# Optimization experiments

Hardware: AMD Instinct MI355X
Metric: run time of the kernel (lower is better)

Reference implementation:

```python
import jax, jax.numpy as jnp
import numpy as np

B, L, D = 2, 4096, 128      # batch, seq_len, d_model
ED = 2 * D                  # d_inner (expand=2) = 256
N = 16                      # d_state
K = 4                       # d_conv
R = (D + 15) // 16          # dt_rank = 8
H = 2 * D                   # mlp hidden = 256


def setup_inputs() -> dict:
    key = jax.random.key(0)
    ks = jax.random.split(key, 20)
    s = 0.05
    inp = {
        "x": jax.random.normal(ks[0], (B, L, D), dtype=jnp.float32),
        # outer block LayerNorm (norm1)
        "norm1_g": jnp.ones((D,), jnp.float32),
        "norm1_b": jnp.zeros((D,), jnp.float32),
        # MambaLayer inner LayerNorm
        "inner_g": jnp.ones((D,), jnp.float32),
        "inner_b": jnp.zeros((D,), jnp.float32),
        # Mamba params
        "in_w": jax.random.normal(ks[1], (2 * ED, D), jnp.float32) * s,      # in_proj (no bias)
        "conv_w": jax.random.normal(ks[2], (ED, 1, K), jnp.float32) * s,     # depthwise conv
        "conv_b": jax.random.normal(ks[3], (ED,), jnp.float32) * s,
        "xproj_w": jax.random.normal(ks[4], (R + 2 * N, ED), jnp.float32) * s,  # x_proj (no bias)
        "dt_w": jax.random.normal(ks[5], (ED, R), jnp.float32) * s,
        "dt_b": jax.random.normal(ks[6], (ED,), jnp.float32) * s,
        "A_log": jnp.tile(jnp.log(jnp.arange(1, N + 1, dtype=jnp.float32)), (ED, 1)),  # [ED,N]
        "Dp": jnp.ones((ED,), jnp.float32),
        "out_w": jax.random.normal(ks[7], (D, ED), jnp.float32) * s,         # out_proj (no bias)
        # MLP
        "fc1_w": jax.random.normal(ks[8], (H, D), jnp.float32) * s,
        "fc1_b": jnp.zeros((H,), jnp.float32),
        "fc2_w": jax.random.normal(ks[9], (D, H), jnp.float32) * s,
        "fc2_b": jnp.zeros((D,), jnp.float32),
    }
    return inp


def _ln(x, g, b, eps=1e-5):
    m = jnp.mean(x, axis=-1, keepdims=True)
    v = jnp.mean((x - m) ** 2, axis=-1, keepdims=True)
    return (x - m) * jax.lax.rsqrt(v + eps) * g + b


def _mamba(x, in_w, conv_w, conv_b, xproj_w, dt_w, dt_b, A_log, Dp, out_w):
    # x: [B, L, D]
    xz = jnp.einsum('bld,ed->ble', x, in_w)          # [B,L,2*ED]
    u, z = jnp.split(xz, 2, axis=-1)                 # each [B,L,ED]
    # causal depthwise conv1d over L
    u_c = jnp.transpose(u, (0, 2, 1))                # [B,ED,L]
    u_c = jax.lax.conv_general_dilated(
        u_c, conv_w, window_strides=(1,), padding=[(K - 1, 0)],
        dimension_numbers=('NCH', 'OIH', 'NCH'), feature_group_count=ED)
    u = jax.nn.silu(jnp.transpose(u_c, (0, 2, 1)) + conv_b)   # [B,L,ED]
    # input-dependent dt, B, C
    dbc = jnp.einsum('ble,re->blr', u, xproj_w)      # [B,L,R+2N]
    dt, Bm, Cm = jnp.split(dbc, [R, R + N], axis=-1)
    delta = jax.nn.softplus(jnp.einsum('blr,er->ble', dt, dt_w) + dt_b)  # [B,L,ED]
    A = -jnp.exp(A_log)                              # [ED,N]
    deltaA = jnp.exp(jnp.einsum('ble,en->blen', delta, A))               # [B,L,ED,N]
    deltaBu = jnp.einsum('ble,bln,ble->blen', delta, Bm, u)              # [B,L,ED,N]
    # selective scan over L
    def step(h, inp):
        dA, dBu, Ct = inp                            # [B,ED,N],[B,ED,N],[B,N]
        h = dA * h + dBu
        y = jnp.einsum('ben,bn->be', h, Ct)
        return h, y
    h0 = jnp.zeros((B, ED, N), u.dtype)
    xs = (jnp.transpose(deltaA, (1, 0, 2, 3)),
          jnp.transpose(deltaBu, (1, 0, 2, 3)),
          jnp.transpose(Cm, (1, 0, 2)))
    _, ys = jax.lax.scan(step, h0, xs)               # [L,B,ED]
    y = jnp.transpose(ys, (1, 0, 2)) + u * Dp        # [B,L,ED]
    y = y * jax.nn.silu(z)
    return jnp.einsum('ble,de->bld', y, out_w)       # [B,L,D]


def reference(x, norm1_g, norm1_b, inner_g, inner_b, in_w, conv_w, conv_b,
              xproj_w, dt_w, dt_b, A_log, Dp, out_w, fc1_w, fc1_b, fc2_w, fc2_b):
    # attn branch: mamba(inner_LN(norm1(x)))
    a = _mamba(_ln(_ln(x, norm1_g, norm1_b), inner_g, inner_b),
               in_w, conv_w, conv_b, xproj_w, dt_w, dt_b, A_log, Dp, out_w)
    x = x + a
    # mlp branch (note: original applies norm1 again to updated x)
    h = _ln(x, norm1_g, norm1_b)
    h = jax.nn.gelu(jnp.einsum('bld,hd->blh', h, fc1_w) + fc1_b, approximate=False)
    h = jnp.einsum('blh,dh->bld', h, fc2_w) + fc2_b
    return x + h
```

## Files before the change

kernel.cpp:

```cpp
#include <hip/hip_runtime.h>
#include <hip/hip_bf16.h>
#include <math.h>

#define BB 2
#define LL 4096
#define DD 128
#define ED 256
#define NN 16
#define KK 4
#define RR 8
#define HH 256
#define NT (BB*LL)
#define NC 128
#define LC 32

typedef __attribute__((ext_vector_type(8))) short short8;
typedef __attribute__((ext_vector_type(8))) unsigned short ushort8v;
typedef __attribute__((ext_vector_type(4))) float floatx4;

__device__ __forceinline__ unsigned short f2bf(float f) {
  unsigned int b = __builtin_bit_cast(unsigned int, f);
  b += 0x7FFFu + ((b >> 16) & 1u);
  return (unsigned short)(b >> 16);
}

__device__ __forceinline__ ushort8v pack8(const float4& v0, const float4& v1) {
  ushort8v p;
  p[0]=f2bf(v0.x); p[1]=f2bf(v0.y); p[2]=f2bf(v0.z); p[3]=f2bf(v0.w);
  p[4]=f2bf(v1.x); p[5]=f2bf(v1.y); p[6]=f2bf(v1.z); p[7]=f2bf(v1.w);
  return p;
}

__global__ __launch_bounds__(256) void gemm_inln_k(const float* __restrict__ x,
    const float* __restrict__ g1, const float* __restrict__ b1,
    const float* __restrict__ g2, const float* __restrict__ b2,
    const float* __restrict__ W, float* __restrict__ C) {
  __shared__ unsigned short As[64][136];
  __shared__ unsigned short Ws[64][136];
  const int row0 = blockIdx.y * 64;
  const int col0 = blockIdx.x * 64;
  const int tid  = threadIdx.x;
  const int wave = tid >> 6, lane = tid & 63;
  const int quad = lane >> 4, l16 = lane & 15;
  const int wm = (wave & 1) * 32, wn = (wave >> 1) * 32;
  const int lr = tid >> 2;
  const int lk = (tid & 3) * 32;

  {
    const float* Ap = x + (size_t)(row0 + lr)*DD + lk;
    float4 av[8];
    float s = 0.f, sq = 0.f;
    #pragma unroll
    for (int g = 0; g < 8; g++) {
      av[g] = *(const float4*)(Ap + g*4);
      s  += av[g].x + av[g].y + av[g].z + av[g].w;
      sq += av[g].x*av[g].x + av[g].y*av[g].y + av[g].z*av[g].z + av[g].w*av[g].w;
    }
    s += __shfl_xor(s, 1);  s += __shfl_xor(s, 2);
    sq += __shfl_xor(sq, 1); sq += __shfl_xor(sq, 2);
    const float m1 = s * (1.f/128.f);
    const float rs1 = rsqrtf(sq*(1.f/128.f) - m1*m1 + 1e-5f);
    float s2 = 0.f, sq2 = 0.f;
    #pragma unroll
    for (int g = 0; g < 8; g++) {
      const float4 gg = *(const float4*)(g1 + lk + g*4);
      const float4 bb = *(const float4*)(b1 + lk + g*4);
      av[g].x = (av[g].x - m1)*rs1*gg.x + bb.x;
      av[g].y = (av[g].y - m1)*rs1*gg.y + bb.y;
      av[g].z = (av[g].z - m1)*rs1*gg.z + bb.z;
      av[g].w = (av[g].w - m1)*rs1*gg.w + bb.w;
      s2  += av[g].x + av[g].y + av[g].z + av[g].w;
      sq2 += av[g].x*av[g].x + av[g].y*av[g].y + av[g].z*av[g].z + av[g].w*av[g].w;
    }
    s2 += __shfl_xor(s2, 1);  s2 += __shfl_xor(s2, 2);
    sq2 += __shfl_xor(sq2, 1); sq2 += __shfl_xor(sq2, 2);
    const float m2 = s2 * (1.f/128.f);
    const float rs2 = rsqrtf(sq2*(1.f/128.f) - m2*m2 + 1e-5f);
    #pragma unroll
    for (int g = 0; g < 4; g++) {
      const float4 ga = *(const float4*)(g2 + lk + g*8);
      const float4 gb = *(const float4*)(g2 + lk + g*8 + 4);
      const float4 ba = *(const float4*)(b2 + lk + g*8);
      const float4 bbv= *(const float4*)(b2 + lk + g*8 + 4);
      ushort8v pa;
      pa[0] = f2bf((av[2*g].x   - m2)*rs2*ga.x + ba.x);
      pa[1] = f2bf((av[2*g].y   - m2)*rs2*ga.y + ba.y);
      pa[2] = f2bf((av[2*g].z   - m2)*rs2*ga.z + ba.z);
      pa[3] = f2bf((av[2*g].w   - m2)*rs2*ga.w + ba.w);
      pa[4] = f2bf((av[2*g+1].x - m2)*rs2*gb.x + bbv.x);
      pa[5] = f2bf((av[2*g+1].y - m2)*rs2*gb.y + bbv.y);
      pa[6] = f2bf((av[2*g+1].z - m2)*rs2*gb.z + bbv.z);
      pa[7] = f2bf((av[2*g+1].w - m2)*rs2*gb.w + bbv.w);
      *(ushort8v*)&As[lr][lk + g*8] = pa;
    }
  }
  {
    const float* Wp = W + (size_t)(col0 + lr)*DD + lk;
    #pragma unroll
    for (int g = 0; g < 4; g++) {
      const float4 v0 = *(const float4*)(Wp + g*8);
      const float4 v1 = *(const float4*)(Wp + g*8 + 4);
      *(ushort8v*)&Ws[lr][lk + g*8] = pack8(v0, v1);
    }
  }
  __syncthreads();

  floatx4 acc[2][2] = {};
  #pragma unroll
  for (int ks = 0; ks < 4; ks++) {
    const int ko = ks*32 + quad*8;
    short8 a0 = *(const short8*)&As[wm +      l16][ko];
    short8 a1 = *(const short8*)&As[wm + 16 + l16][ko];
    short8 b0 = *(const short8*)&Ws[wn +      l16][ko];
    short8 b1 = *(const short8*)&Ws[wn + 16 + l16][ko];
    acc[0][0] = __builtin_amdgcn_mfma_f32_16x16x32_bf16(a0, b0, acc[0][0], 0, 0, 0);
    acc[0][1] = __builtin_amdgcn_mfma_f32_16x16x32_bf16(a0, b1, acc[0][1], 0, 0, 0);
    acc[1][0] = __builtin_amdgcn_mfma_f32_16x16x32_bf16(a1, b0, acc[1][0], 0, 0, 0);
    acc[1][1] = __builtin_amdgcn_mfma_f32_16x16x32_bf16(a1, b1, acc[1][1], 0, 0, 0);
  }
  #pragma unroll
  for (int i = 0; i < 2; i++)
    #pragma unroll
    for (int j = 0; j < 2; j++) {
      const int n = col0 + wn + j*16 + l16;
      #pragma unroll
      for (int r = 0; r < 4; r++) {
        const int m = row0 + wm + i*16 + quad*4 + r;
        C[(size_t)m*(2*ED) + n] = acc[i][j][r];
      }
    }
}

__global__ __launch_bounds__(256) void scan1f_k(
    const float* __restrict__ xz, const float* __restrict__ cw,
    const float* __restrict__ cb, const float* __restrict__ xpw,
    const float* __restrict__ dtw, const float* __restrict__ dtb,
    const float* __restrict__ A_log, float* __restrict__ uc,
    float* __restrict__ dbc, float* __restrict__ delta,
    float* __restrict__ cA, float* __restrict__ cH) {
  __shared__ __align__(16) unsigned short Bs[64][264];
  __shared__ __align__(16) unsigned short As[32][264];
  __shared__ float su[32][128];
  __shared__ float sdbc[32][40];
  float (*sdel)[128] = reinterpret_cast<float(*)[128]>(&As[0][0]);

  const int eb = blockIdx.x, c = blockIdx.y, b = blockIdx.z;
  const int tid = threadIdx.x;
  const int t0 = b*LL + c*LC;

  #pragma unroll
  for (int p = 0; p < 8; p++) {
    const int idx = p*256 + tid;
    const int row = idx >> 5;
    const int col = (idx & 31) * 8;
    ushort8v v = {};
    if (row < 40) {
      const float4 v0 = *(const float4*)(xpw + (size_t)row*ED + col);
      const float4 v1 = *(const float4*)(xpw + (size_t)row*ED + col + 4);
      v = pack8(v0, v1);
    }
    *(ushort8v*)&Bs[row][col] = v;
  }

  {
    const int ch = tid;
    const float4 w = *(const float4*)(cw + ch*4);
    const float cbe = cb[ch];
    float h0 = 0.f, h1 = 0.f, h2 = 0.f;
    if (c != 0) {
      h0 = xz[(size_t)(t0-3)*(2*ED) + ch];
      h1 = xz[(size_t)(t0-2)*(2*ED) + ch];
      h2 = xz[(size_t)(t0-1)*(2*ED) + ch];
    }
    const bool own = (ch >> 7) == eb;
    #pragma unroll 8
    for (int i = 0; i < LC; i++) {
      const float cur = xz[(size_t)(t0+i)*(2*ED) + ch];
      const float a = cbe + h0*w.x + h1*w.y + h2*w.z + cur*w.w;
      const float s = a / (1.f + __expf(-a));
      As[i][ch] = f2bf(s);
      if (own) {
        su[i][ch & 127] = s;
        uc[(size_t)(t0+i)*ED + ch] = s;
      }
      h0 = h1; h1 = h2; h2 = cur;
    }
  }
  __syncthreads();

  const int wave = tid >> 6, lane = tid & 63;
  const int quad = lane >> 4, l16 = lane & 15;
  {
    const int mi = (wave & 1) * 16;
    const int j0 = (wave >> 1) * 2;
    floatx4 acc[2] = {};
    #pragma unroll
    for (int ks = 0; ks < 8; ks++) {
      const int ko = ks*32 + quad*8;
      short8 a  = *(const short8*)&As[mi + l16][ko];
      short8 b0 = *(const short8*)&Bs[j0*16 +      l16][ko];
      short8 b1 = *(const short8*)&Bs[j0*16 + 16 + l16][ko];
      acc[0] = __builtin_amdgcn_mfma_f32_16x16x32_bf16(a, b0, acc[0], 0, 0, 0);
      acc[1] = __builtin_amdgcn_mfma_f32_16x16x32_bf16(a, b1, acc[1], 0, 0, 0);
    }
    __syncthreads();
    #pragma unroll
    for (int f = 0; f < 2; f++) {
      const int n = (j0 + f)*16 + l16;
      #pragma unroll
      for (int r = 0; r < 4; r++) {
        const int m = mi + quad*4 + r;
        if (n < 40) {
          sdbc[m][n] = acc[f][r];
          if (eb == 0) dbc[(size_t)(t0 + m)*40 + n] = acc[f][r];
        }
      }
    }
  }
  __syncthreads();

  const int e_loc = tid >> 1;
  const int half  = tid & 1;
  const int e     = eb*128 + e_loc;
  {
    const float4 w0 = *(const float4*)(dtw + e*RR);
    const float4 w1 = *(const float4*)(dtw + e*RR + 4);
    const float db = dtb[e];
    #pragma unroll 4
    for (int i = 0; i < 16; i++) {
      const int t = half*16 + i;
      const float a = db
          + sdbc[t][0]*w0.x + sdbc[t][1]*w0.y + sdbc[t][2]*w0.z + sdbc[t][3]*w0.w
          + sdbc[t][4]*w1.x + sdbc[t][5]*w1.y + sdbc[t][6]*w1.z + sdbc[t][7]*w1.w;
      const float d = (a > 20.f) ? a : log1pf(__expf(a));
      sdel[t][e_loc] = d;
      delta[(size_t)(t0+t)*ED + e] = d;
    }
  }
  __syncthreads();

  const int n0 = half * 8;
  const float4 a0 = *(const float4*)(A_log + e*NN + n0);
  const float4 a1 = *(const float4*)(A_log + e*NN + n0 + 4);
  float Aen[8] = {-__expf(a0.x), -__expf(a0.y), -__expf(a0.z), -__expf(a0.w),
                  -__expf(a1.x), -__expf(a1.y), -__expf(a1.z), -__expf(a1.w)};
  float h[8] = {};
  float sumd = 0.f;
  for (int i = 0; i < LC; i++) {
    const float dv = sdel[i][e_loc];
    const float du = dv * su[i][e_loc];
    const float4 B0 = *(const float4*)&sdbc[i][RR + n0];
    const float4 B1 = *(const float4*)&sdbc[i][RR + n0 + 4];
    const float Bv[8] = {B0.x,B0.y,B0.z,B0.w,B1.x,B1.y,B1.z,B1.w};
    sumd += dv;
    #pragma unroll
    for (int j = 0; j < 8; j++)
      h[j] = __expf(dv * Aen[j])*h[j] + Bv[j]*du;
  }
  const size_t base = (((size_t)c*BB + b)*ED + e)*NN + n0;
  *(float4*)(cA + base)     = make_float4(__expf(sumd*Aen[0]), __expf(sumd*Aen[1]),
                                          __expf(sumd*Aen[2]), __expf(sumd*Aen[3]));
  *(float4*)(cA + base + 4) = make_float4(__expf(sumd*Aen[4]), __expf(sumd*Aen[5]),
                                          __expf(sumd*Aen[6]), __expf(sumd*Aen[7]));
  *(float4*)(cH + base)     = make_float4(h[0], h[1], h[2], h[3]);
  *(float4*)(cH + base + 4) = make_float4(h[4], h[5], h[6], h[7]);
}

__global__ __launch_bounds__(256) void scan2_k(float* __restrict__ cA,
    const float* __restrict__ cH) {
  const int gt = blockIdx.x*256 + threadIdx.x;
  const int b = gt >> 12;
  const size_t base = (size_t)b*ED*NN + (gt & 4095);
  float h = 0.f;
  for (int g = 0; g < NC/16; g++) {
    float av[16], hv[16];
    #pragma unroll
    for (int i = 0; i < 16; i++) {
      const size_t idx = (size_t)(g*16 + i)*(BB*ED*NN) + base;
      av[i] = cA[idx]; hv[i] = cH[idx];
    }
    #pragma unroll
    for (int i = 0; i < 16; i++) {
      const size_t idx = (size_t)(g*16 + i)*(BB*ED*NN) + base;
      cA[idx] = h;
      h = av[i]*h + hv[i];
    }
  }
}

__global__ __launch_bounds__(256, 1) void tail_k(
    const float* __restrict__ xz, const float* __restrict__ delta,
    const float* __restrict__ uc, const float* __restrict__ dbc,
    const float* __restrict__ cP, const float* __restrict__ A_log,
    const float* __restrict__ Dpv, const float* __restrict__ x,
    const float* __restrict__ g1, const float* __restrict__ b1,
    const float* __restrict__ out_w, const float* __restrict__ fc1_w,
    const float* __restrict__ fc1_b, const float* __restrict__ fc2_w,
    const float* __restrict__ fc2_b, float* __restrict__ out) {
  __shared__ __align__(16) unsigned short BigW[34816];
  __shared__ __align__(16) unsigned short Au[32][264];
  __shared__ float xs[32][132];
  __shared__ float sbc[32][32];

  const int c = blockIdx.x, b = blockIdx.y;
  const int t0 = b*LL + c*LC;
  const int tid = threadIdx.x;
  const int wave = tid >> 6, lane = tid & 63;
  const int quad = lane >> 4, l16 = lane & 15;

  #pragma unroll
  for (int p = 0; p < 4; p++) {
    const int idx = p*256 + tid;
    const int row = idx >> 5, col = idx & 31;
    sbc[row][col] = dbc[(size_t)(t0 + row)*40 + RR + col];
  }

  {
    const int e = tid;
    float Aen[16], h[16];
    #pragma unroll
    for (int g = 0; g < 4; g++) {
      const float4 a = *(const float4*)(A_log + e*NN + g*4);
      Aen[4*g]=-__expf(a.x); Aen[4*g+1]=-__expf(a.y);
      Aen[4*g+2]=-__expf(a.z); Aen[4*g+3]=-__expf(a.w);
      const float4 hp = *(const float4*)(cP + (((size_t)c*BB + b)*ED + e)*NN + g*4);
      h[4*g]=hp.x; h[4*g+1]=hp.y; h[4*g+2]=hp.z; h[4*g+3]=hp.w;
    }
    const float Dpe = Dpv[e];
    __syncthreads();
    #pragma unroll 4
    for (int i = 0; i < LC; i++) {
      const float dv = delta[(size_t)(t0+i)*ED + e];
      const float uv = uc[(size_t)(t0+i)*ED + e];
      const float du = dv * uv;
      float part = 0.f;
      #pragma unroll
      for (int j = 0; j < 16; j++) {
        h[j] = __expf(dv * Aen[j])*h[j] + sbc[i][j]*du;
        part += h[j]*sbc[i][16+j];
      }
      const float zv = xz[(size_t)(t0+i)*(2*ED) + ED + e];
      const float g = zv / (1.f + __expf(-zv));
      Au[i][e] = f2bf((part + uv*Dpe) * g);
    }
  }
  {
    const int r = tid >> 1, k0 = (tid & 1) * 128;
    const float* wp = out_w + (size_t)r*ED + k0;
    #pragma unroll
    for (int g = 0; g < 16; g++) {
      const float4 v0 = *(const float4*)(wp + g*8);
      const float4 v1 = *(const float4*)(wp + g*8 + 4);
      *(ushort8v*)&BigW[(size_t)r*264 + k0 + g*8] = pack8(v0, v1);
    }
  }
  __syncthreads();

  {
    const int wn = wave * 32;
    floatx4 acc[2][2] = {};
    #pragma unroll
    for (int ks = 0; ks < 8; ks++) {
      const int ko = ks*32 + quad*8;
      short8 a0 = *(const short8*)&Au[l16][ko];
      short8 a1 = *(const short8*)&Au[16 + l16][ko];
      short8 b0 = *(const short8*)&BigW[(size_t)(wn +      l16)*264 + ko];
      short8 b1 = *(const short8*)&BigW[(size_t)(wn + 16 + l16)*264 + ko];
      acc[0][0] = __builtin_amdgcn_mfma_f32_16x16x32_bf16(a0, b0, acc[0][0], 0, 0, 0);
      acc[0][1] = __builtin_amdgcn_mfma_f32_16x16x32_bf16(a0, b1, acc[0][1], 0, 0, 0);
      acc[1][0] = __builtin_amdgcn_mfma_f32_16x16x32_bf16(a1, b0, acc[1][0], 0, 0, 0);
      acc[1][1] = __builtin_amdgcn_mfma_f32_16x16x32_bf16(a1, b1, acc[1][1], 0, 0, 0);
    }
    #pragma unroll
    for (int i = 0; i < 2; i++)
      #pragma unroll
      for (int j = 0; j < 2; j++) {
        const int n = wn + j*16 + l16;
        #pragma unroll
        for (int r = 0; r < 4; r++) {
          const int m = i*16 + quad*4 + r;
          xs[m][n] = acc[i][j][r] + x[(size_t)(t0 + m)*DD + n];
        }
      }
  }
  __syncthreads();

  {
    const int lr = tid >> 3, le = (tid & 7) * 16;
    float vv[16];
    float s = 0.f, sq = 0.f;
    #pragma unroll
    for (int i = 0; i < 16; i++) {
      vv[i] = xs[lr][le + i];
      s += vv[i]; sq += vv[i]*vv[i];
    }
    s += __shfl_xor(s, 1);  s += __shfl_xor(s, 2);  s += __shfl_xor(s, 4);
    sq += __shfl_xor(sq, 1); sq += __shfl_xor(sq, 2); sq += __shfl_xor(sq, 4);
    const float mean = s * (1.f/128.f);
    const float rs = rsqrtf(sq*(1.f/128.f) - mean*mean + 1e-5f);
    #pragma unroll
    for (int g = 0; g < 2; g++) {
      ushort8v p;
      #pragma unroll
      for (int i = 0; i < 8; i++) {
        const int idx = g*8 + i;
        p[i] = f2bf((vv[idx] - mean)*rs*g1[le + idx] + b1[le + idx]);
      }
      *(ushort8v*)&Au[lr][le + g*8] = p;
    }
  }
  {
    const float* wp = fc1_w + (size_t)tid*DD;
    #pragma unroll
    for (int g = 0; g < 16; g++) {
      const float4 v0 = *(const float4*)(wp + g*8);
      const float4 v1 = *(const float4*)(wp + g*8 + 4);
      *(ushort8v*)&BigW[(size_t)tid*136 + g*8] = pack8(v0, v1);
    }
  }
  __syncthreads();

  {
    const int wn = wave * 64;
    floatx4 acc[2][4] = {};
    #pragma unroll
    for (int ks = 0; ks < 4; ks++) {
      const int ko = ks*32 + quad*8;
      short8 a0 = *(const short8*)&Au[l16][ko];
      short8 a1 = *(const short8*)&Au[16 + l16][ko];
      #pragma unroll
      for (int f = 0; f < 4; f++) {
        short8 bv = *(const short8*)&BigW[(size_t)(wn + f*16 + l16)*136 + ko];
        acc[0][f] = __builtin_amdgcn_mfma_f32_16x16x32_bf16(a0, bv, acc[0][f], 0, 0, 0);
        acc[1][f] = __builtin_amdgcn_mfma_f32_16x16x32_bf16(a1, bv, acc[1][f], 0, 0, 0);
      }
    }
    __syncthreads();
    #pragma unroll
    for (int i = 0; i < 2; i++)
      #pragma unroll
      for (int f = 0; f < 4; f++) {
        const int n = wn + f*16 + l16;
        const float bn = fc1_b[n];
        #pragma unroll
        for (int r = 0; r < 4; r++) {
          const int m = i*16 + quad*4 + r;
          float v = acc[i][f][r] + bn;
          v = 0.5f*v*(1.f + erff(v*0.70710678118f));
          Au[m][n] = f2bf(v);
        }
      }
  }
  {
    const int r = tid >> 1, k0 = (tid & 1) * 128;
    const float* wp = fc2_w + (size_t)r*HH + k0;
    __syncthreads();
    #pragma unroll
    for (int g = 0; g < 16; g++) {
      const float4 v0 = *(const float4*)(wp + g*8);
      const float4 v1 = *(const float4*)(wp + g*8 + 4);
      *(ushort8v*)&BigW[(size_t)r*264 + k0 + g*8] = pack8(v0, v1);
    }
  }
  __syncthreads();

  {
    const int wn = wave * 32;
    floatx4 acc[2][2] = {};
    #pragma unroll
    for (int ks = 0; ks < 8; ks++) {
      const int ko = ks*32 + quad*8;
      short8 a0 = *(const short8*)&Au[l16][ko];
      short8 a1 = *(const short8*)&Au[16 + l16][ko];
      short8 b0 = *(const short8*)&BigW[(size_t)(wn +      l16)*264 + ko];
      short8 b1 = *(const short8*)&BigW[(size_t)(wn + 16 + l16)*264 + ko];
      acc[0][0] = __builtin_amdgcn_mfma_f32_16x16x32_bf16(a0, b0, acc[0][0], 0, 0, 0);
      acc[0][1] = __builtin_amdgcn_mfma_f32_16x16x32_bf16(a0, b1, acc[0][1], 0, 0, 0);
      acc[1][0] = __builtin_amdgcn_mfma_f32_16x16x32_bf16(a1, b0, acc[1][0], 0, 0, 0);
      acc[1][1] = __builtin_amdgcn_mfma_f32_16x16x32_bf16(a1, b1, acc[1][1], 0, 0, 0);
    }
    #pragma unroll
    for (int i = 0; i < 2; i++)
      #pragma unroll
      for (int j = 0; j < 2; j++) {
        const int n = wn + j*16 + l16;
        const float bn = fc2_b[n];
        #pragma unroll
        for (int r = 0; r < 4; r++) {
          const int m = i*16 + quad*4 + r;
          out[(size_t)(t0 + m)*DD + n] = acc[i][j][r] + bn + xs[m][n];
        }
      }
  }
}

extern "C" void kernel_launch(void* const* d_in, const int* in_sizes, int n_in,
                              void* d_out, int out_size, void* d_ws, size_t ws_size,
                              hipStream_t stream) {
  const float* x      = (const float*)d_in[0];
  const float* n1g    = (const float*)d_in[1];
  const float* n1b    = (const float*)d_in[2];
  const float* ing    = (const float*)d_in[3];
  const float* inb    = (const float*)d_in[4];
  const float* in_w   = (const float*)d_in[5];
  const float* conv_w = (const float*)d_in[6];
  const float* conv_b = (const float*)d_in[7];
  const float* xproj_w= (const float*)d_in[8];
  const float* dt_w   = (const float*)d_in[9];
  const float* dt_b   = (const float*)d_in[10];
  const float* A_log  = (const float*)d_in[11];
  const float* Dpv    = (const float*)d_in[12];
  const float* out_w  = (const float*)d_in[13];
  const float* fc1_w  = (const float*)d_in[14];
  const float* fc1_b  = (const float*)d_in[15];
  const float* fc2_w  = (const float*)d_in[16];
  const float* fc2_b  = (const float*)d_in[17];
  float* out = (float*)d_out;

  float* ws    = (float*)d_ws;
  float* xz    = ws;
  float* uc    = xz    + (size_t)NT*2*ED;
  float* dbc   = uc    + (size_t)NT*ED;
  float* delta = dbc   + (size_t)NT*40;
  float* cAP   = delta + (size_t)NT*ED;
  float* cH    = cAP   + (size_t)NC*BB*ED*NN;

  gemm_inln_k<<<dim3(512/64, NT/64), 256, 0, stream>>>(x, n1g, n1b, ing, inb, in_w, xz);
  scan1f_k<<<dim3(2, NC, BB), 256, 0, stream>>>(xz, conv_w, conv_b, xproj_w, dt_w, dt_b,
                                                A_log, uc, dbc, delta, cAP, cH);
  scan2_k<<<(BB*ED*NN)/256, 256, 0, stream>>>(cAP, cH);
  tail_k<<<dim3(NC, BB), 256, 0, stream>>>(xz, delta, uc, dbc, cAP, A_log, Dpv,
                                           x, n1g, n1b, out_w, fc1_w, fc1_b,
                                           fc2_w, fc2_b, out);
}
```

Measured before the change: 188.7 us.

## Split tail kernel into half-chunk blocks with recomputed scan prefix

The tail kernel now launches twice as many blocks, each handling 16 tokens instead of 32. Odd blocks recompute the first 16 steps of the chunk scan without output so their hidden state is correct. Weight staging in shared memory is cut to 128x136 tiles loaded in K halves, which shrinks LDS and allows two blocks per CU. This trades redundant scan work and extra weight reloads and barriers for more parallelism and occupancy across CUs.

Measured after the change: 199.2 us. 1.06x slower.

```diff
diff --git a/kernel.cpp b/kernel.cpp
--- a/kernel.cpp
+++ b/kernel.cpp
@@ -288,7 +288,7 @@
   }
 }
 
-__global__ __launch_bounds__(256, 1) void tail_k(
+__global__ __launch_bounds__(256, 2) void tail2_k(
     const float* __restrict__ xz, const float* __restrict__ delta,
     const float* __restrict__ uc, const float* __restrict__ dbc,
     const float* __restrict__ cP, const float* __restrict__ A_log,
@@ -297,22 +297,25 @@
     const float* __restrict__ out_w, const float* __restrict__ fc1_w,
     const float* __restrict__ fc1_b, const float* __restrict__ fc2_w,
     const float* __restrict__ fc2_b, float* __restrict__ out) {
-  __shared__ __align__(16) unsigned short BigW[34816];
-  __shared__ __align__(16) unsigned short Au[32][264];
-  __shared__ float xs[32][132];
+  __shared__ __align__(16) unsigned short BigW[128*136];
+  __shared__ __align__(16) unsigned short Au[16][264];
+  __shared__ float xs[16][132];
   __shared__ float sbc[32][32];
 
-  const int c = blockIdx.x, b = blockIdx.y;
-  const int t0 = b*LL + c*LC;
+  const int c2 = blockIdx.x, b = blockIdx.y;
+  const int c = c2 >> 1, odd = c2 & 1;
+  const int tc0 = b*LL + c*LC;
+  const int t0  = b*LL + c2*16;
   const int tid = threadIdx.x;
   const int wave = tid >> 6, lane = tid & 63;
   const int quad = lane >> 4, l16 = lane & 15;
+  const int wn = wave * 32;
 
   #pragma unroll
   for (int p = 0; p < 4; p++) {
     const int idx = p*256 + tid;
     const int row = idx >> 5, col = idx & 31;
-    sbc[row][col] = dbc[(size_t)(t0 + row)*40 + RR + col];
+    sbc[row][col] = dbc[(size_t)(tc0 + row)*40 + RR + col];
   }
 
   {
@@ -328,169 +331,160 @@
     }
     const float Dpe = Dpv[e];
     __syncthreads();
+    if (odd) {
+      #pragma unroll 4
+      for (int i = 0; i < 16; i++) {
+        const float dv = delta[(size_t)(tc0+i)*ED + e];
+        const float du = dv * uc[(size_t)(tc0+i)*ED + e];
+        #pragma unroll
+        for (int j = 0; j < 16; j++)
+          h[j] = __expf(dv * Aen[j])*h[j] + sbc[i][j]*du;
+      }
+    }
+    const int ib = odd * 16;
     #pragma unroll 4
-    for (int i = 0; i < LC; i++) {
+    for (int i = 0; i < 16; i++) {
       const float dv = delta[(size_t)(t0+i)*ED + e];
       const float uv = uc[(size_t)(t0+i)*ED + e];
       const float du = dv * uv;
       float part = 0.f;
       #pragma unroll
       for (int j = 0; j < 16; j++) {
-        h[j] = __expf(dv * Aen[j])*h[j] + sbc[i][j]*du;
-        part += h[j]*sbc[i][16+j];
+        h[j] = __expf(dv * Aen[j])*h[j] + sbc[ib+i][j]*du;
+        part += h[j]*sbc[ib+i][16+j];
       }
       const float zv = xz[(size_t)(t0+i)*(2*ED) + ED + e];
       const float g = zv / (1.f + __expf(-zv));
       Au[i][e] = f2bf((part + uv*Dpe) * g);
     }
   }
-  {
-    const int r = tid >> 1, k0 = (tid & 1) * 128;
-    const float* wp = out_w + (size_t)r*ED + k0;
-    #pragma unroll
-    for (int g = 0; g < 16; g++) {
+
+  {
+    floatx4 acc[2] = {};
+    for (int ks0 = 0; ks0 < ED; ks0 += 128) {
+      __syncthreads();
+      const int r = tid >> 1, k0 = (tid & 1) * 64;
+      const float* wp = out_w + (size_t)r*ED + ks0 + k0;
+      #pragma unroll
+      for (int g = 0; g < 8; g++) {
+        const float4 v0 = *(const float4*)(wp + g*8);
+        const float4 v1 = *(const float4*)(wp + g*8 + 4);
+        *(ushort8v*)&BigW[r*136 + k0 + g*8] = pack8(v0, v1);
+      }
+      __syncthreads();
+      #pragma unroll
+      for (int ks = 0; ks < 4; ks++) {
+        const int ko = ks*32 + quad*8;
+        short8 a  = *(const short8*)&Au[l16][ks0 + ko];
+        short8 b0 = *(const short8*)&BigW[(wn +      l16)*136 + ko];
+        short8 b1 = *(const short8*)&BigW[(wn + 16 + l16)*136 + ko];
+        acc[0] = __builtin_amdgcn_mfma_f32_16x16x32_bf16(a, b0, acc[0], 0, 0, 0);
+        acc[1] = __builtin_amdgcn_mfma_f32_16x16x32_bf16(a, b1, acc[1], 0, 0, 0);
+      }
+    }
+    #pragma unroll
+    for (int j = 0; j < 2; j++) {
+      const int n = wn + j*16 + l16;
+      #pragma unroll
+      for (int r = 0; r < 4; r++) {
+        const int m = quad*4 + r;
+        xs[m][n] = acc[j][r] + x[(size_t)(t0 + m)*DD + n];
+      }
+    }
+  }
+  __syncthreads();
+
+  {
+    const int lr = tid >> 4, le = (tid & 15) * 8;
+    float vv[8];
+    float s = 0.f, sq = 0.f;
+    #pragma unroll
+    for (int i = 0; i < 8; i++) {
+      vv[i] = xs[lr][le + i];
+      s += vv[i]; sq += vv[i]*vv[i];
+    }
+    s += __shfl_xor(s, 1);  s += __shfl_xor(s, 2);
+    s += __shfl_xor(s, 4);  s += __shfl_xor(s, 8);
+    sq += __shfl_xor(sq, 1); sq += __shfl_xor(sq, 2);
+    sq += __shfl_xor(sq, 4); sq += __shfl_xor(sq, 8);
+    const float mean = s * (1.f/128.f);
+    const float rs = rsqrtf(sq*(1.f/128.f) - mean*mean + 1e-5f);
+    ushort8v p;
+    #pragma unroll
+    for (int i = 0; i < 8; i++)
+      p[i] = f2bf((vv[i] - mean)*rs*g1[le + i] + b1[le + i]);
+    *(ushort8v*)&Au[lr][le] = p;
+  }
+
+  for (int hh = 1; hh >= 0; hh--) {
+    __syncthreads();
+    const int rr = tid >> 1, k0 = (tid & 1) * 64;
+    const float* wp = fc1_w + (size_t)(hh*128 + rr)*DD + k0;
+    #pragma unroll
+    for (int g = 0; g < 8; g++) {
       const float4 v0 = *(const float4*)(wp + g*8);
       const float4 v1 = *(const float4*)(wp + g*8 + 4);
-      *(ushort8v*)&BigW[(size_t)r*264 + k0 + g*8] = pack8(v0, v1);
-    }
-  }
-  __syncthreads();
-
-  {
-    const int wn = wave * 32;
-    floatx4 acc[2][2] = {};
-    #pragma unroll
-    for (int ks = 0; ks < 8; ks++) {
-      const int ko = ks*32 + quad*8;
-      short8 a0 = *(const short8*)&Au[l16][ko];
-      short8 a1 = *(const short8*)&Au[16 + l16][ko];
-      short8 b0 = *(const short8*)&BigW[(size_t)(wn +      l16)*264 + ko];
-      short8 b1 = *(const short8*)&BigW[(size_t)(wn + 16 + l16)*264 + ko];
-      acc[0][0] = __builtin_amdgcn_mfma_f32_16x16x32_bf16(a0, b0, acc[0][0], 0, 0, 0);
-      acc[0][1] = __builtin_amdgcn_mfma_f32_16x16x32_bf16(a0, b1, acc[0][1], 0, 0, 0);
-      acc[1][0] = __builtin_amdgcn_mfma_f32_16x16x32_bf16(a1, b0, acc[1][0], 0, 0, 0);
-      acc[1][1] = __builtin_amdgcn_mfma_f32_16x16x32_bf16(a1, b1, acc[1][1], 0, 0, 0);
-    }
-    #pragma unroll
-    for (int i = 0; i < 2; i++)
-      #pragma unroll
-      for (int j = 0; j < 2; j++) {
-        const int n = wn + j*16 + l16;
-        #pragma unroll
-        for (int r = 0; r < 4; r++) {
-          const int m = i*16 + quad*4 + r;
-          xs[m][n] = acc[i][j][r] + x[(size_t)(t0 + m)*DD + n];
-        }
-      }
-  }
-  __syncthreads();
-
-  {
-    const int lr = tid >> 3, le = (tid & 7) * 16;
-    float vv[16];
-    float s = 0.f, sq = 0.f;
-    #pragma unroll
-    for (int i = 0; i < 16; i++) {
-      vv[i] = xs[lr][le + i];
-      s += vv[i]; sq += vv[i]*vv[i];
-    }
-    s += __shfl_xor(s, 1);  s += __shfl_xor(s, 2);  s += __shfl_xor(s, 4);
-    sq += __shfl_xor(sq, 1); sq += __shfl_xor(sq, 2); sq += __shfl_xor(sq, 4);
-    const float mean = s * (1.f/128.f);
-    const float rs = rsqrtf(sq*(1.f/128.f) - mean*mean + 1e-5f);
-    #pragma unroll
-    for (int g = 0; g < 2; g++) {
-      ushort8v p;
-      #pragma unroll
-      for (int i = 0; i < 8; i++) {
-        const int idx = g*8 + i;
-        p[i] = f2bf((vv[idx] - mean)*rs*g1[le + idx] + b1[le + idx]);
-      }
-      *(ushort8v*)&Au[lr][le + g*8] = p;
-    }
-  }
-  {
-    const float* wp = fc1_w + (size_t)tid*DD;
-    #pragma unroll
-    for (int g = 0; g < 16; g++) {
-      const float4 v0 = *(const float4*)(wp + g*8);
-      const float4 v1 = *(const float4*)(wp + g*8 + 4);
-      *(ushort8v*)&BigW[(size_t)tid*136 + g*8] = pack8(v0, v1);
-    }
-  }
-  __syncthreads();
-
-  {
-    const int wn = wave * 64;
-    floatx4 acc[2][4] = {};
+      *(ushort8v*)&BigW[rr*136 + k0 + g*8] = pack8(v0, v1);
+    }
+    __syncthreads();
+    floatx4 acc[2] = {};
     #pragma unroll
     for (int ks = 0; ks < 4; ks++) {
       const int ko = ks*32 + quad*8;
-      short8 a0 = *(const short8*)&Au[l16][ko];
-      short8 a1 = *(const short8*)&Au[16 + l16][ko];
-      #pragma unroll
-      for (int f = 0; f < 4; f++) {
-        short8 bv = *(const short8*)&BigW[(size_t)(wn + f*16 + l16)*136 + ko];
-        acc[0][f] = __builtin_amdgcn_mfma_f32_16x16x32_bf16(a0, bv, acc[0][f], 0, 0, 0);
-        acc[1][f] = __builtin_amdgcn_mfma_f32_16x16x32_bf16(a1, bv, acc[1][f], 0, 0, 0);
-      }
-    }
-    __syncthreads();
-    #pragma unroll
-    for (int i = 0; i < 2; i++)
-      #pragma unroll
-      for (int f = 0; f < 4; f++) {
-        const int n = wn + f*16 + l16;
-        const float bn = fc1_b[n];
-        #pragma unroll
-        for (int r = 0; r < 4; r++) {
-          const int m = i*16 + quad*4 + r;
-          float v = acc[i][f][r] + bn;
-          v = 0.5f*v*(1.f + erff(v*0.70710678118f));
-          Au[m][n] = f2bf(v);
-        }
-      }
-  }
-  {
-    const int r = tid >> 1, k0 = (tid & 1) * 128;
-    const float* wp = fc2_w + (size_t)r*HH + k0;
-    __syncthreads();
-    #pragma unroll
-    for (int g = 0; g < 16; g++) {
-      const float4 v0 = *(const float4*)(wp + g*8);
-      const float4 v1 = *(const float4*)(wp + g*8 + 4);
-      *(ushort8v*)&BigW[(size_t)r*264 + k0 + g*8] = pack8(v0, v1);
-    }
-  }
-  __syncthreads();
-
-  {
-    const int wn = wave * 32;
-    floatx4 acc[2][2] = {};
-    #pragma unroll
-    for (int ks = 0; ks < 8; ks++) {
-      const int ko = ks*32 + quad*8;
-      short8 a0 = *(const short8*)&Au[l16][ko];
-      short8 a1 = *(const short8*)&Au[16 + l16][ko];
-      short8 b0 = *(const short8*)&BigW[(size_t)(wn +      l16)*264 + ko];
-      short8 b1 = *(const short8*)&BigW[(size_t)(wn + 16 + l16)*264 + ko];
-      acc[0][0] = __builtin_amdgcn_mfma_f32_16x16x32_bf16(a0, b0, acc[0][0], 0, 0, 0);
-      acc[0][1] = __builtin_amdgcn_mfma_f32_16x16x32_bf16(a0, b1, acc[0][1], 0, 0, 0);
-      acc[1][0] = __builtin_amdgcn_mfma_f32_16x16x32_bf16(a1, b0, acc[1][0], 0, 0, 0);
-      acc[1][1] = __builtin_amdgcn_mfma_f32_16x16x32_bf16(a1, b1, acc[1][1], 0, 0, 0);
-    }
-    #pragma unroll
-    for (int i = 0; i < 2; i++)
-      #pragma unroll
-      for (int j = 0; j < 2; j++) {
-        const int n = wn + j*16 + l16;
-        const float bn = fc2_b[n];
-        #pragma unroll
-        for (int r = 0; r < 4; r++) {
-          const int m = i*16 + quad*4 + r;
-          out[(size_t)(t0 + m)*DD + n] = acc[i][j][r] + bn + xs[m][n];
-        }
-      }
+      short8 a  = *(const short8*)&Au[l16][ko];
+      short8 b0 = *(const short8*)&BigW[(wn +      l16)*136 + ko];
+      short8 b1 = *(const short8*)&BigW[(wn + 16 + l16)*136 + ko];
+      acc[0] = __builtin_amdgcn_mfma_f32_16x16x32_bf16(a, b0, acc[0], 0, 0, 0);
+      acc[1] = __builtin_amdgcn_mfma_f32_16x16x32_bf16(a, b1, acc[1], 0, 0, 0);
+    }
+    if (hh == 0) __syncthreads();
+    #pragma unroll
+    for (int j = 0; j < 2; j++) {
+      const int n = wn + j*16 + l16;
+      const float bn = fc1_b[hh*128 + n];
+      #pragma unroll
+      for (int r = 0; r < 4; r++) {
+        const int m = quad*4 + r;
+        float v = acc[j][r] + bn;
+        v = 0.5f*v*(1.f + erff(v*0.70710678118f));
+        Au[m][hh*128 + n] = f2bf(v);
+      }
+    }
+  }
+
+  {
+    floatx4 acc[2] = {};
+    for (int ks0 = 0; ks0 < HH; ks0 += 128) {
+      __syncthreads();
+      const int r = tid >> 1, k0 = (tid & 1) * 64;
+      const float* wp = fc2_w + (size_t)r*HH + ks0 + k0;
+      #pragma unroll
+      for (int g = 0; g < 8; g++) {
+        const float4 v0 = *(const float4*)(wp + g*8);
+        const float4 v1 = *(const float4*)(wp + g*8 + 4);
+        *(ushort8v*)&BigW[r*136 + k0 + g*8] = pack8(v0, v1);
+      }
+      __syncthreads();
+      #pragma unroll
+      for (int ks = 0; ks < 4; ks++) {
+        const int ko = ks*32 + quad*8;
+        short8 a  = *(const short8*)&Au[l16][ks0 + ko];
+        short8 b0 = *(const short8*)&BigW[(wn +      l16)*136 + ko];
+        short8 b1 = *(const short8*)&BigW[(wn + 16 + l16)*136 + ko];
+        acc[0] = __builtin_amdgcn_mfma_f32_16x16x32_bf16(a, b0, acc[0], 0, 0, 0);
+        acc[1] = __builtin_amdgcn_mfma_f32_16x16x32_bf16(a, b1, acc[1], 0, 0, 0);
+      }
+    }
+    #pragma unroll
+    for (int j = 0; j < 2; j++) {
+      const int n = wn + j*16 + l16;
+      const float bn = fc2_b[n];
+      #pragma unroll
+      for (int r = 0; r < 4; r++) {
+        const int m = quad*4 + r;
+        out[(size_t)(t0 + m)*DD + n] = acc[j][r] + bn + xs[m][n];
+      }
+    }
   }
 }
 
@@ -529,7 +523,7 @@
   scan1f_k<<<dim3(2, NC, BB), 256, 0, stream>>>(xz, conv_w, conv_b, xproj_w, dt_w, dt_b,
                                                 A_log, uc, dbc, delta, cAP, cH);
   scan2_k<<<(BB*ED*NN)/256, 256, 0, stream>>>(cAP, cH);
-  tail_k<<<dim3(NC, BB), 256, 0, stream>>>(xz, delta, uc, dbc, cAP, A_log, Dpv,
-                                           x, n1g, n1b, out_w, fc1_w, fc1_b,
-                                           fc2_w, fc2_b, out);
-}
+  tail2_k<<<dim3(2*NC, BB), 256, 0, stream>>>(xz, delta, uc, dbc, cAP, A_log, Dpv,
+                                              x, n1g, n1b, out_w, fc1_w, fc1_b,
+                                              fc2_w, fc2_b, out);
+}
```

## Prefetch scan inputs in registers, read B/C directly, shrink scan2 blocks

Applied to the files above, without the earlier changes.

In scan1f the 32 conv inputs are loaded into registers up front so the loads are not serialized inside the recurrence. The tail kernel now stages out_w into LDS before the scan, double-buffers delta/u/z loads in 8-step register groups, and reads B/C as float4 vectors straight from global memory instead of through an LDS tile and barrier. scan2 uses 128-thread blocks to spread the small carry pass over more CUs. Register pressure rises and the B/C reads are repeated per thread, relying on cache hits.

New measurement: 188.0 us (median of 2 runs). About the same (-0.4%).

```diff
diff --git a/kernel.cpp b/kernel.cpp
--- a/kernel.cpp
+++ b/kernel.cpp
@@ -166,6 +166,10 @@
     const int ch = tid;
     const float4 w = *(const float4*)(cw + ch*4);
     const float cbe = cb[ch];
+    float xv[32];
+    #pragma unroll
+    for (int i = 0; i < LC; i++)
+      xv[i] = xz[(size_t)(t0+i)*(2*ED) + ch];
     float h0 = 0.f, h1 = 0.f, h2 = 0.f;
     if (c != 0) {
       h0 = xz[(size_t)(t0-3)*(2*ED) + ch];
@@ -173,9 +177,9 @@
       h2 = xz[(size_t)(t0-1)*(2*ED) + ch];
     }
     const bool own = (ch >> 7) == eb;
-    #pragma unroll 8
+    #pragma unroll
     for (int i = 0; i < LC; i++) {
-      const float cur = xz[(size_t)(t0+i)*(2*ED) + ch];
+      const float cur = xv[i];
       const float a = cbe + h0*w.x + h1*w.y + h2*w.z + cur*w.w;
       const float s = a / (1.f + __expf(-a));
       As[i][ch] = f2bf(s);
@@ -266,9 +270,9 @@
   *(float4*)(cH + base + 4) = make_float4(h[4], h[5], h[6], h[7]);
 }
 
-__global__ __launch_bounds__(256) void scan2_k(float* __restrict__ cA,
+__global__ __launch_bounds__(128) void scan2_k(float* __restrict__ cA,
     const float* __restrict__ cH) {
-  const int gt = blockIdx.x*256 + threadIdx.x;
+  const int gt = blockIdx.x*128 + threadIdx.x;
   const int b = gt >> 12;
   const size_t base = (size_t)b*ED*NN + (gt & 4095);
   float h = 0.f;
@@ -288,7 +292,7 @@
   }
 }
 
-__global__ __launch_bounds__(256, 1) void tail_k(
+__global__ __launch_bounds__(256, 1) void tail4_k(
     const float* __restrict__ xz, const float* __restrict__ delta,
     const float* __restrict__ uc, const float* __restrict__ dbc,
     const float* __restrict__ cP, const float* __restrict__ A_log,
@@ -300,7 +304,6 @@
   __shared__ __align__(16) unsigned short BigW[34816];
   __shared__ __align__(16) unsigned short Au[32][264];
   __shared__ float xs[32][132];
-  __shared__ float sbc[32][32];
 
   const int c = blockIdx.x, b = blockIdx.y;
   const int t0 = b*LL + c*LC;
@@ -308,11 +311,15 @@
   const int wave = tid >> 6, lane = tid & 63;
   const int quad = lane >> 4, l16 = lane & 15;
 
-  #pragma unroll
-  for (int p = 0; p < 4; p++) {
-    const int idx = p*256 + tid;
-    const int row = idx >> 5, col = idx & 31;
-    sbc[row][col] = dbc[(size_t)(t0 + row)*40 + RR + col];
+  {
+    const int r = tid >> 1, k0 = (tid & 1) * 128;
+    const float* wp = out_w + (size_t)r*ED + k0;
+    #pragma unroll
+    for (int g = 0; g < 16; g++) {
+      const float4 v0 = *(const float4*)(wp + g*8);
+      const float4 v1 = *(const float4*)(wp + g*8 + 4);
+      *(ushort8v*)&BigW[(size_t)r*264 + k0 + g*8] = pack8(v0, v1);
+    }
   }
 
   {
@@ -327,31 +334,54 @@
       h[4*g]=hp.x; h[4*g+1]=hp.y; h[4*g+2]=hp.z; h[4*g+3]=hp.w;
     }
     const float Dpe = Dpv[e];
-    __syncthreads();
-    #pragma unroll 4
-    for (int i = 0; i < LC; i++) {
-      const float dv = delta[(size_t)(t0+i)*ED + e];
-      const float uv = uc[(size_t)(t0+i)*ED + e];
-      const float du = dv * uv;
-      float part = 0.f;
-      #pragma unroll
-      for (int j = 0; j < 16; j++) {
-        h[j] = __expf(dv * Aen[j])*h[j] + sbc[i][j]*du;
-        part += h[j]*sbc[i][16+j];
-      }
-      const float zv = xz[(size_t)(t0+i)*(2*ED) + ED + e];
-      const float g = zv / (1.f + __expf(-zv));
-      Au[i][e] = f2bf((part + uv*Dpe) * g);
-    }
-  }
-  {
-    const int r = tid >> 1, k0 = (tid & 1) * 128;
-    const float* wp = out_w + (size_t)r*ED + k0;
-    #pragma unroll
-    for (int g = 0; g < 16; g++) {
-      const float4 v0 = *(const float4*)(wp + g*8);
-      const float4 v1 = *(const float4*)(wp + g*8 + 4);
-      *(ushort8v*)&BigW[(size_t)r*264 + k0 + g*8] = pack8(v0, v1);
+    float pd[8], pu[8], pz[8];
+    #pragma unroll
+    for (int i = 0; i < 8; i++) {
+      pd[i] = delta[(size_t)(t0+i)*ED + e];
+      pu[i] = uc[(size_t)(t0+i)*ED + e];
+      pz[i] = xz[(size_t)(t0+i)*(2*ED) + ED + e];
+    }
+    for (int g4 = 0; g4 < 4; g4++) {
+      float cd[8], cu[8], cz[8];
+      #pragma unroll
+      for (int i = 0; i < 8; i++) { cd[i]=pd[i]; cu[i]=pu[i]; cz[i]=pz[i]; }
+      if (g4 < 3) {
+        const int tn = t0 + (g4+1)*8;
+        #pragma unroll
+        for (int i = 0; i < 8; i++) {
+          pd[i] = delta[(size_t)(tn+i)*ED + e];
+          pu[i] = uc[(size_t)(tn+i)*ED + e];
+          pz[i] = xz[(size_t)(tn+i)*(2*ED) + ED + e];
+        }
+      }
+      #pragma unroll
+      for (int i = 0; i < 8; i++) {
+        const int t = g4*8 + i;
+        const float dv = cd[i];
+        const float uv = cu[i];
+        const float du = dv * uv;
+        const float* bc = dbc + (size_t)(t0 + t)*40 + RR;
+        const float4 B0 = *(const float4*)(bc);
+        const float4 B1 = *(const float4*)(bc + 4);
+        const float4 B2 = *(const float4*)(bc + 8);
+        const float4 B3 = *(const float4*)(bc + 12);
+        const float4 C0 = *(const float4*)(bc + 16);
+        const float4 C1 = *(const float4*)(bc + 20);
+        const float4 C2 = *(const float4*)(bc + 24);
+        const float4 C3 = *(const float4*)(bc + 28);
+        const float Bv[16] = {B0.x,B0.y,B0.z,B0.w, B1.x,B1.y,B1.z,B1.w,
+                              B2.x,B2.y,B2.z,B2.w, B3.x,B3.y,B3.z,B3.w};
+        const float Cv[16] = {C0.x,C0.y,C0.z,C0.w, C1.x,C1.y,C1.z,C1.w,
+                              C2.x,C2.y,C2.z,C2.w, C3.x,C3.y,C3.z,C3.w};
+        float part = 0.f;
+        #pragma unroll
+        for (int j = 0; j < 16; j++) {
+          h[j] = __expf(dv * Aen[j])*h[j] + Bv[j]*du;
+          part += h[j]*Cv[j];
+        }
+        const float g = cz[i] / (1.f + __expf(-cz[i]));
+        Au[t][e] = f2bf((part + uv*Dpe) * g);
+      }
     }
   }
   __syncthreads();
@@ -528,8 +558,8 @@
   gemm_inln_k<<<dim3(512/64, NT/64), 256, 0, stream>>>(x, n1g, n1b, ing, inb, in_w, xz);
   scan1f_k<<<dim3(2, NC, BB), 256, 0, stream>>>(xz, conv_w, conv_b, xproj_w, dt_w, dt_b,
                                                 A_log, uc, dbc, delta, cAP, cH);
-  scan2_k<<<(BB*ED*NN)/256, 256, 0, stream>>>(cAP, cH);
-  tail_k<<<dim3(NC, BB), 256, 0, stream>>>(xz, delta, uc, dbc, cAP, A_log, Dpv,
-                                           x, n1g, n1b, out_w, fc1_w, fc1_b,
-                                           fc2_w, fc2_b, out);
-}
+  scan2_k<<<(BB*ED*NN)/128, 128, 0, stream>>>(cAP, cH);
+  tail4_k<<<dim3(NC, BB), 256, 0, stream>>>(xz, delta, uc, dbc, cAP, A_log, Dpv,
+                                            x, n1g, n1b, out_w, fc1_w, fc1_b,
+                                            fc2_w, fc2_b, out);
+}
```
